# Optimization experiments

Measured on AMD Instinct MI355X. Metric: run time of the kernel, lower is better.

## Reference

```python
import jax, jax.numpy as jnp
import numpy as np
import math

H = 8  # num_heads
SCALE = 1.0 / math.sqrt(512.0)  # original divides by sqrt(dim_V), not sqrt(head_dim)


def setup_inputs() -> dict:
    key = jax.random.key(0)
    ks = jax.random.split(key, 16)
    B, N, D = 32, 512, 512
    s = 1.0 / math.sqrt(D)
    return {
        "Q": jax.random.normal(ks[0], (B, N, D), jnp.float32),
        "K": jax.random.normal(ks[1], (B, N, D), jnp.float32),
        "Wq": jax.random.normal(ks[2], (D, D), jnp.float32) * s,
        "bq": jnp.zeros((D,), jnp.float32),
        "Wk": jax.random.normal(ks[3], (D, D), jnp.float32) * s,
        "bk": jnp.zeros((D,), jnp.float32),
        "Wv": jax.random.normal(ks[4], (D, D), jnp.float32) * s,
        "bv": jnp.zeros((D,), jnp.float32),
        "Wo": jax.random.normal(ks[5], (D, D), jnp.float32) * s,
        "bo": jnp.zeros((D,), jnp.float32),
        "W1": jax.random.normal(ks[6], (D, D), jnp.float32) * s,
        "b1": jnp.zeros((D,), jnp.float32),
        "W2": jax.random.normal(ks[7], (D, D), jnp.float32) * s,
        "b2": jnp.zeros((D,), jnp.float32),
    }


def reference(Q, K, Wq, bq, Wk, bk, Wv, bv, Wo, bo, W1, b1, W2, b2):
    B, Nq, D = Q.shape
    dh = D // H
    # projections (torch Linear: x @ W.T + b)
    q = (Q @ Wq.T + bq).reshape(B, Nq, H, dh)
    k = (K @ Wk.T + bk).reshape(B, K.shape[1], H, dh)
    v = (K @ Wv.T + bv).reshape(B, K.shape[1], H, dh)
    # scores: [B, H, Nq, Nk], scaled by 1/sqrt(dim_V)
    scores = jnp.einsum("bqhd,bkhd->bhqk", q, k) * SCALE
    # NOTE: original softmax is over dim=1 of [H*B, Nq, Nk] == the QUERY axis
    A = jax.nn.softmax(scores, axis=2)
    attn = jnp.einsum("bhqk,bkhd->bqhd", A, v).reshape(B, Nq, D)
    out = Q + (attn @ Wo.T + bo)  # dropout p=0.0
    ffn = jax.nn.relu(out @ W1.T + b1) @ W2.T + b2
    return out + ffn
```

## Files before the change

kernel.cpp:

```cpp
#include <hip/hip_runtime.h>
#include <stdint.h>

#define SCALE_ 0.044194173824159216f
#define QSC_ (0.044194173824159216f * 1.4426950408889634f)

typedef __attribute__((ext_vector_type(8))) short bf16x8;
typedef __attribute__((ext_vector_type(4))) float f32x4;
typedef __attribute__((ext_vector_type(16))) float f32x16;
typedef __attribute__((ext_vector_type(2))) unsigned int uint2v;

__device__ __forceinline__ ushort f2b(float f) {
  union { float f; uint32_t u; } v; v.f = f;
  return (ushort)((v.u + 0x7fffu + ((v.u >> 16) & 1u)) >> 16);
}
__device__ __forceinline__ uint32_t cvtpk(float lo, float hi) {
  uint32_t r; asm("v_cvt_pk_bf16_f32 %0, %1, %2" : "=v"(r) : "v"(lo), "v"(hi)); return r;
}
__device__ __forceinline__ float ex2(float x) {
  float r; asm("v_exp_f32 %0, %1" : "=v"(r) : "v"(x)); return r;
}
__device__ __forceinline__ void gld16(void* lds, const void* g) {
  __builtin_amdgcn_global_load_lds(
      (const __attribute__((address_space(1))) uint32_t*)g,
      (__attribute__((address_space(3))) uint32_t*)lds, 16, 0, 0);
}

__global__ __launch_bounds__(256)
void k_cvtw(const float* __restrict__ w0, const float* __restrict__ w1,
            const float* __restrict__ w2, const float* __restrict__ w3,
            const float* __restrict__ w4, const float* __restrict__ w5,
            ushort* __restrict__ Wb)
{
  const int NW = 262144;
  int i = (blockIdx.x * 256 + threadIdx.x) * 4;
  int seg = i >> 18;
  int off = i & (NW - 1);
  const float* src;
  switch (seg) { case 0: src = w0; break; case 1: src = w1; break; case 2: src = w2; break;
                 case 3: src = w3; break; case 4: src = w4; break; default: src = w5; }
  float4 v = *(const float4*)(src + off);
  ushort4 o = make_ushort4(f2b(v.x), f2b(v.y), f2b(v.z), f2b(v.w));
  *(ushort4*)(Wb + (size_t)seg * NW + off) = o;
}

template<int EPI>
__device__ __forceinline__ void gemm_body(const ushort* __restrict__ A, const ushort* __restrict__ Bw,
                                          const float* __restrict__ bias, const float* __restrict__ extra,
                                          float* __restrict__ outf, ushort* __restrict__ outb,
                                          char* lds, int m0, int n0)
{
  const int t = threadIdx.x;
  const int w = t >> 6, lane = t & 63;
  const int wm = w >> 1, wn = w & 1;
  const int rA = lane & 15, g = lane >> 4;

  const ushort* srcA[4]; int ldsA[4];
#pragma unroll
  for (int j = 0; j < 4; j++) {
    int L = (t + j*512) * 16;
    int U = L ^ (((L >> 7) & 7) << 4);
    srcA[j] = A + (size_t)(m0 + (U >> 7))*512 + ((U & 127) >> 1);
    ldsA[j] = L;
  }
  const ushort* srcB[2]; int ldsB[2];
#pragma unroll
  for (int j = 0; j < 2; j++) {
    int L = (t + j*512) * 16;
    int U = L ^ (((L >> 7) & 7) << 4);
    srcB[j] = Bw + (size_t)(n0 + (U >> 7))*512 + ((U & 127) >> 1);
    ldsB[j] = 32768 + L;
  }

#define STAGE_A(ti) do { char* bb_ = lds + ((ti) % 3) * 49152; \
    _Pragma("unroll") \
    for (int j = 0; j < 4; j++) gld16(bb_ + ldsA[j], srcA[j] + (ti)*64); } while (0)
#define STAGE_B(ti) do { char* bb_ = lds + ((ti) % 3) * 49152; \
    _Pragma("unroll") \
    for (int j = 0; j < 2; j++) gld16(bb_ + ldsB[j], srcB[j] + (ti)*64); } while (0)

  STAGE_A(0); STAGE_B(0);
  STAGE_A(1); STAGE_B(1);

  f32x4 acc[4][4] = {};
  for (int i = 0; i < 8; i++) {
    if (i < 7) asm volatile("s_waitcnt vmcnt(6)" ::: "memory");
    else       asm volatile("s_waitcnt vmcnt(0)" ::: "memory");
    __builtin_amdgcn_s_barrier();
    __builtin_amdgcn_sched_barrier(0);
    const char* bufc = lds + (i % 3) * 49152;

    bf16x8 afA[4], bfA[4], afB[4], bfB[4];
#pragma unroll
    for (int m = 0; m < 4; m++) {
      int row = wm*64 + m*16 + rA;
      afA[m] = *(const bf16x8*)(bufc + ((row*128 + g*16) ^ ((row & 7) << 4)));
      afB[m] = *(const bf16x8*)(bufc + ((row*128 + 64 + g*16) ^ ((row & 7) << 4)));
    }
#pragma unroll
    for (int n = 0; n < 4; n++) {
      int row = wn*64 + n*16 + rA;
      bfA[n] = *(const bf16x8*)(bufc + 32768 + ((row*128 + g*16) ^ ((row & 7) << 4)));
      bfB[n] = *(const bf16x8*)(bufc + 32768 + ((row*128 + 64 + g*16) ^ ((row & 7) << 4)));
    }
    if (i < 6) { STAGE_A(i + 2); STAGE_B(i + 2); }
    __builtin_amdgcn_sched_barrier(0);
    __builtin_amdgcn_s_setprio(1);
#pragma unroll
    for (int m = 0; m < 4; m++)
#pragma unroll
      for (int n = 0; n < 4; n++)
        acc[m][n] = __builtin_amdgcn_mfma_f32_16x16x32_bf16(afA[m], bfA[n], acc[m][n], 0, 0, 0);
#pragma unroll
    for (int m = 0; m < 4; m++)
#pragma unroll
      for (int n = 0; n < 4; n++)
        acc[m][n] = __builtin_amdgcn_mfma_f32_16x16x32_bf16(afB[m], bfB[n], acc[m][n], 0, 0, 0);
    __builtin_amdgcn_s_setprio(0);
  }
#undef STAGE_A
#undef STAGE_B

#pragma unroll
  for (int m = 0; m < 4; m++)
#pragma unroll
    for (int n = 0; n < 4; n++) {
      int col = n0 + wn*64 + n*16 + rA;
      float bb = bias[col];
#pragma unroll
      for (int r = 0; r < 4; r++) {
        int row = m0 + wm*64 + m*16 + g*4 + r;
        size_t idx = (size_t)row*512 + col;
        float v = acc[m][n][r] + bb;
        if (EPI == 1)      { float o = extra[idx] + v; outf[idx] = o; outb[idx] = f2b(o); }
        else if (EPI == 2) outb[idx] = f2b(v > 0.f ? v : 0.f);
        else               outf[idx] += v;
      }
    }
}

template<int EPI>
__global__ __launch_bounds__(512, 2)
void k_gemm(const ushort* __restrict__ A, const ushort* __restrict__ Bw,
            const float* __restrict__ bias, const float* __restrict__ extra,
            float* __restrict__ outf, ushort* __restrict__ outb)
{
  __shared__ __align__(16) char lds[3*49152];
  gemm_body<EPI>(A, Bw, bias, extra, outf, outb, lds, blockIdx.x*256, blockIdx.y*128);
}

template<int EPI>
__device__ __forceinline__ void gemm_f32a_body(const float* __restrict__ A32, const ushort* __restrict__ Bw,
                                               const float* __restrict__ bias,
                                               float* __restrict__ outf, ushort* __restrict__ outb,
                                               char* lds, int m0, int n0, float os)
{
  const int t = threadIdx.x;
  const int w = t >> 6, lane = t & 63;
  const int wm = w >> 1, wn = w & 1;
  const int rA = lane & 15, g = lane >> 4;

  const float* srcA[4]; int ldsA[4];
#pragma unroll
  for (int j = 0; j < 4; j++) {
    int L = (t + j*512) * 16;
    int U = L ^ (((L >> 7) & 7) << 4);
    srcA[j] = A32 + (size_t)(m0 + (U >> 7))*512 + ((U & 127) >> 1);
    ldsA[j] = L;
  }
  const ushort* srcB[2]; int ldsB[2];
#pragma unroll
  for (int j = 0; j < 2; j++) {
    int L = (t + j*512) * 16;
    int U = L ^ (((L >> 7) & 7) << 4);
    srcB[j] = Bw + (size_t)(n0 + (U >> 7))*512 + ((U & 127) >> 1);
    ldsB[j] = 32768 + L;
  }

#define QLA(ti, R) do { \
    _Pragma("unroll") \
    for (int j = 0; j < 4; j++) { \
      R[2*j]   = *(const float4*)(srcA[j] + (ti)*64); \
      R[2*j+1] = *(const float4*)(srcA[j] + (ti)*64 + 4); } } while (0)
#define QWA(ti, R) do { char* bb_ = lds + ((ti) % 3) * 49152; \
    _Pragma("unroll") \
    for (int j = 0; j < 4; j++) { \
      uint4 qq; \
      qq.x = cvtpk(R[2*j].x,   R[2*j].y); \
      qq.y = cvtpk(R[2*j].z,   R[2*j].w); \
      qq.z = cvtpk(R[2*j+1].x, R[2*j+1].y); \
      qq.w = cvtpk(R[2*j+1].z, R[2*j+1].w); \
      *(uint4*)(bb_ + ldsA[j]) = qq; } } while (0)
#define QSB(ti) do { char* bb_ = lds + ((ti) % 3) * 49152; \
    _Pragma("unroll") \
    for (int j = 0; j < 2; j++) gld16(bb_ + ldsB[j], srcB[j] + (ti)*64); } while (0)

  float4 a0[8], a1[8], a2[8];
  QSB(0);
  QLA(0, a0);
  QLA(1, a1);
  QLA(2, a2);
  QSB(1);
  __builtin_amdgcn_sched_barrier(0);
  asm volatile("s_waitcnt vmcnt(18)" ::: "memory");
  QWA(0, a0);

  f32x4 acc[4][4] = {};

#define QITER(i, RW, RL) do { \
    if ((i) <= 5)      asm volatile("s_waitcnt vmcnt(10) lgkmcnt(0)" ::: "memory"); \
    else if ((i) == 6) asm volatile("s_waitcnt vmcnt(2) lgkmcnt(0)" ::: "memory"); \
    else               asm volatile("s_waitcnt vmcnt(0) lgkmcnt(0)" ::: "memory"); \
    __builtin_amdgcn_s_barrier(); \
    __builtin_amdgcn_sched_barrier(0); \
    if ((i) < 7) QWA((i) + 1, RW); \
    __builtin_amdgcn_sched_barrier(0); \
    const char* bufc = lds + ((i) % 3) * 49152; \
    bf16x8 afA[4], bfA[4]; \
    _Pragma("unroll") \
    for (int m = 0; m < 4; m++) { \
      int row = wm*64 + m*16 + rA; \
      afA[m] = *(const bf16x8*)(bufc + ((row*128 + g*16) ^ ((row & 7) << 4))); \
    } \
    _Pragma("unroll") \
    for (int n = 0; n < 4; n++) { \
      int row = wn*64 + n*16 + rA; \
      bfA[n] = *(const bf16x8*)(bufc + 32768 + ((row*128 + g*16) ^ ((row & 7) << 4))); \
    } \
    if ((i) < 5) QLA((i) + 3, RL); \
    if ((i) < 6) QSB((i) + 2); \
    __builtin_amdgcn_sched_barrier(0); \
    __builtin_amdgcn_s_setprio(1); \
    _Pragma("unroll") \
    for (int m = 0; m < 4; m++) \
      _Pragma("unroll") \
      for (int n = 0; n < 4; n++) \
        acc[m][n] = __builtin_amdgcn_mfma_f32_16x16x32_bf16(afA[m], bfA[n], acc[m][n], 0, 0, 0); \
    __builtin_amdgcn_s_setprio(0); \
    bf16x8 afB[4], bfB[4]; \
    _Pragma("unroll") \
    for (int m = 0; m < 4; m++) { \
      int row = wm*64 + m*16 + rA; \
      afB[m] = *(const bf16x8*)(bufc + ((row*128 + 64 + g*16) ^ ((row & 7) << 4))); \
    } \
    _Pragma("unroll") \
    for (int n = 0; n < 4; n++) { \
      int row = wn*64 + n*16 + rA; \
      bfB[n] = *(const bf16x8*)(bufc + 32768 + ((row*128 + 64 + g*16) ^ ((row & 7) << 4))); \
    } \
    __builtin_amdgcn_s_setprio(1); \
    _Pragma("unroll") \
    for (int m = 0; m < 4; m++) \
      _Pragma("unroll") \
      for (int n = 0; n < 4; n++) \
        acc[m][n] = __builtin_amdgcn_mfma_f32_16x16x32_bf16(afB[m], bfB[n], acc[m][n], 0, 0, 0); \
    __builtin_amdgcn_s_setprio(0); \
  } while (0)

  QITER(0, a1, a0);
  QITER(1, a2, a1);
  QITER(2, a0, a2);
  QITER(3, a1, a0);
  QITER(4, a2, a1);
  QITER(5, a0, a2);
  QITER(6, a1, a0);
  QITER(7, a2, a1);
#undef QITER
#undef QLA
#undef QWA
#undef QSB

#pragma unroll
  for (int m = 0; m < 4; m++)
#pragma unroll
    for (int n = 0; n < 4; n++) {
      int col = n0 + wn*64 + n*16 + rA;
      float bb = bias[col];
      if (EPI == 4) {
        int b = m0 >> 9, k0 = m0 & 511;
        int hh = col >> 6, dl = col & 63;
        int kg = k0 + wm*64 + m*16 + g*4;
        float v0 = acc[m][n][0] + bb, v1 = acc[m][n][1] + bb;
        float v2 = acc[m][n][2] + bb, v3 = acc[m][n][3] + bb;
        uint2 pk;
        pk.x = (uint32_t)f2b(v0) | ((uint32_t)f2b(v1) << 16);
        pk.y = (uint32_t)f2b(v2) | ((uint32_t)f2b(v3) << 16);
        *(uint2*)(outb + ((size_t)((b*8 + hh)*64 + dl)*512 + kg)) = pk;
      } else {
#pragma unroll
        for (int r = 0; r < 4; r++) {
          int row = m0 + wm*64 + m*16 + g*4 + r;
          size_t idx = (size_t)row*512 + col;
          outb[idx] = f2b((acc[m][n][r] + bb) * os);
        }
      }
    }
}

__global__ __launch_bounds__(512, 2)
void k_gemm_qkvf(const float* __restrict__ Qf, const float* __restrict__ Kf,
                 const ushort* __restrict__ Wb, const float* __restrict__ bq,
                 const float* __restrict__ bk, const float* __restrict__ bvv,
                 ushort* __restrict__ qkout, ushort* __restrict__ vpT)
{
  __shared__ __align__(16) char lds[3*49152];
  int z = blockIdx.z;
  if (z == 2) {
    gemm_f32a_body<4>(Kf, Wb + 2*(size_t)262144, bvv, nullptr, vpT,
                      lds, blockIdx.x*256, blockIdx.y*128, 1.0f);
  } else if (z == 1) {
    gemm_f32a_body<0>(Kf, Wb + (size_t)262144, bk, nullptr, qkout + (size_t)8388608,
                      lds, blockIdx.x*256, blockIdx.y*128, 1.0f);
  } else {
    gemm_f32a_body<0>(Qf, Wb, bq, nullptr, qkout,
                      lds, blockIdx.x*256, blockIdx.y*128, QSC_);
  }
}

__global__ __launch_bounds__(512, 2)
void k_att2(const ushort* __restrict__ qp, const ushort* __restrict__ kp,
            const ushort* __restrict__ vpT, float* __restrict__ zinv,
            ushort* __restrict__ attn)
{
  __shared__ __align__(16) char kt[65536];
  __shared__ __align__(16) char vt[65536];
  __shared__ __align__(16) char qpr[32768];
  int bh = blockIdx.x;
  int b = bh >> 3, h = bh & 7;
  int t = threadIdx.x, w = t >> 6, lane = t & 63;
  int rA = lane & 15, g = lane >> 4;
  const ushort* kbase = kp + (size_t)(b*512)*512 + h*64;
  const ushort* qbase = qp + (size_t)(b*512)*512 + h*64;
  const ushort* vbase = vpT + (size_t)bh*64*512;

#pragma unroll
  for (int i = 0; i < 8; i++) {
    int c = i*512 + t; int row = c >> 3, sl = c & 7;
    gld16(kt + c*16, kbase + (size_t)row*512 + ((sl ^ (row & 7))*8));
  }
#define STAGE_Q(buf, qb) do { \
    _Pragma("unroll") \
    for (int i = 0; i < 2; i++) { \
      int c = i*512 + t; int row = c >> 3, sl = c & 7; \
      gld16(qpr + (buf)*16384 + c*16, \
            qbase + (size_t)((qb)*128 + row)*512 + ((sl ^ (row & 7))*8)); } } while (0)
  STAGE_Q(0, 0);
  STAGE_Q(1, 1);
#pragma unroll
  for (int i = 0; i < 8; i++) {
    int c = i*512 + t; int d = c >> 6, sl = c & 63;
    gld16(vt + c*16, vbase + (size_t)d*512 + ((sl ^ (d & 7))*8));
  }

  asm volatile("s_waitcnt vmcnt(10)" ::: "memory");
  __builtin_amdgcn_s_barrier();
  __builtin_amdgcn_sched_barrier(0);
  bf16x8 kf[4][2];
#pragma unroll
  for (int n = 0; n < 4; n++)
#pragma unroll
    for (int ks = 0; ks < 2; ks++) {
      int k = w*64 + n*16 + rA;
      kf[n][ks] = *(const bf16x8*)(kt + k*128 + (((ks*4 + g) ^ (k & 7))*16));
    }
  float Zacc[4] = {0.f, 0.f, 0.f, 0.f};
  for (int qb = 0; qb < 4; qb++) {
    if (qb == 1)      { asm volatile("s_waitcnt vmcnt(10)" ::: "memory"); }
    else if (qb == 2) { asm volatile("s_waitcnt vmcnt(2)" ::: "memory"); }
    else if (qb == 3) { asm volatile("s_waitcnt vmcnt(0)" ::: "memory"); }
    if (qb) { __builtin_amdgcn_s_barrier(); __builtin_amdgcn_sched_barrier(0); }
    const char* qtb = qpr + (qb & 1)*16384;
    f32x4 acc[8][4] = {};
#pragma unroll
    for (int ks = 0; ks < 2; ks++) {
      bf16x8 af[8];
#pragma unroll
      for (int m = 0; m < 8; m++) {
        int q = m*16 + rA;
        af[m] = *(const bf16x8*)(qtb + q*128 + (((ks*4 + g) ^ (q & 7))*16));
      }
      __builtin_amdgcn_s_setprio(1);
#pragma unroll
      for (int m = 0; m < 8; m++)
#pragma unroll
        for (int n = 0; n < 4; n++)
          acc[m][n] = __builtin_amdgcn_mfma_f32_16x16x32_bf16(af[m], kf[n][ks], acc[m][n], 0, 0, 0);
      __builtin_amdgcn_s_setprio(0);
    }
    if (qb < 3) __builtin_amdgcn_s_barrier();
    if (qb < 2) STAGE_Q(qb & 1, qb + 2);
#pragma unroll
    for (int m = 0; m < 8; m++)
#pragma unroll
      for (int n = 0; n < 4; n++) {
        float s = 0.f;
#pragma unroll
        for (int r = 0; r < 4; r++) s += ex2(acc[m][n][r]);
        Zacc[n] += s;
      }
  }
#undef STAGE_Q
#pragma unroll
  for (int n = 0; n < 4; n++) {
    float v = Zacc[n];
    v += __shfl_xor(v, 16);
    v += __shfl_xor(v, 32);
    if (lane < 16) ((float*)qpr)[w*64 + n*16 + lane] = 1.0f / v;
  }
  __syncthreads();

  const int l31 = lane & 31, hi5 = lane >> 5;
  bf16x8 qf2[2][4];
#pragma unroll
  for (int qb = 0; qb < 2; qb++)
#pragma unroll
    for (int ksd = 0; ksd < 4; ksd++)
      qf2[qb][ksd] = *(const bf16x8*)(qbase + (size_t)(w*64 + qb*32 + l31)*512 + ksd*16 + hi5*8);
  const float* zl = (const float*)qpr;
  f32x16 oacc[2][2] = {};
  for (int kc = 0; kc < 16; kc++) {
    bf16x8 kf2[4];
#pragma unroll
    for (int ksd = 0; ksd < 4; ksd++) {
      int k = kc*32 + l31;
      kf2[ksd] = *(const bf16x8*)(kt + k*128 + (((ksd*2 + hi5) ^ (k & 7))*16));
    }
    bf16x8 vf2[2][2];
#pragma unroll
    for (int db = 0; db < 2; db++)
#pragma unroll
      for (int ks = 0; ks < 2; ks++) {
        int d = db*32 + l31;
        vf2[db][ks] = *(const bf16x8*)(vt + d*1024 + (((kc*4 + ks*2 + hi5) ^ (d & 7))*16));
      }
    f32x4 zv[4];
#pragma unroll
    for (int j = 0; j < 4; j++)
      zv[j] = *(const f32x4*)(zl + kc*32 + j*8 + hi5*4);
#pragma unroll
    for (int qb = 0; qb < 2; qb++) {
      f32x16 s = {};
      __builtin_amdgcn_s_setprio(1);
#pragma unroll
      for (int ksd = 0; ksd < 4; ksd++)
        s = __builtin_amdgcn_mfma_f32_32x32x16_bf16(kf2[ksd], qf2[qb][ksd], s, 0, 0, 0);
      __builtin_amdgcn_s_setprio(0);
      float e[16];
#pragma unroll
      for (int r = 0; r < 16; r++) e[r] = ex2(s[r]) * zv[r >> 2][r & 3];
      uint32_t x0 = cvtpk(e[0], e[1]),   y0 = cvtpk(e[4], e[5]);
      uint32_t x1 = cvtpk(e[2], e[3]),   y1 = cvtpk(e[6], e[7]);
      uint32_t x2 = cvtpk(e[8], e[9]),   y2 = cvtpk(e[12], e[13]);
      uint32_t x3 = cvtpk(e[10], e[11]), y3 = cvtpk(e[14], e[15]);
      uint2v r0 = __builtin_amdgcn_permlane32_swap(x0, y0, false, false);
      uint2v r1 = __builtin_amdgcn_permlane32_swap(x1, y1, false, false);
      uint2v r2 = __builtin_amdgcn_permlane32_swap(x2, y2, false, false);
      uint2v r3 = __builtin_amdgcn_permlane32_swap(x3, y3, false, false);
      union { uint32_t u[4]; bf16x8 v; } p0, p1;
      p0.u[0] = r0[0]; p0.u[1] = r1[0]; p0.u[2] = r0[1]; p0.u[3] = r1[1];
      p1.u[0] = r2[0]; p1.u[1] = r3[0]; p1.u[2] = r2[1]; p1.u[3] = r3[1];
      __builtin_amdgcn_s_setprio(1);
#pragma unroll
      for (int db = 0; db < 2; db++) {
        oacc[qb][db] = __builtin_amdgcn_mfma_f32_32x32x16_bf16(p0.v, vf2[db][0], oacc[qb][db], 0, 0, 0);
        oacc[qb][db] = __builtin_amdgcn_mfma_f32_32x32x16_bf16(p1.v, vf2[db][1], oacc[qb][db], 0, 0, 0);
      }
      __builtin_amdgcn_s_setprio(0);
    }
  }
#pragma unroll
  for (int qb = 0; qb < 2; qb++)
#pragma unroll
    for (int db = 0; db < 2; db++)
#pragma unroll
      for (int r = 0; r < 16; r++) {
        int q = w*64 + qb*32 + (r & 3) + 8*(r >> 2) + 4*hi5;
        int d = db*32 + l31;
        attn[(size_t)(b*512 + q)*512 + h*64 + d] = f2b(oacc[qb][db][r]);
      }
}

extern "C" void kernel_launch(void* const* d_in, const int* in_sizes, int n_in,
                              void* d_out, int out_size, void* d_ws, size_t ws_size,
                              hipStream_t stream) {
  const float* Q  = (const float*)d_in[0];
  const float* K  = (const float*)d_in[1];
  const float* Wq = (const float*)d_in[2];
  const float* bq = (const float*)d_in[3];
  const float* Wk = (const float*)d_in[4];
  const float* bk = (const float*)d_in[5];
  const float* Wv = (const float*)d_in[6];
  const float* bv = (const float*)d_in[7];
  const float* Wo = (const float*)d_in[8];
  const float* bo = (const float*)d_in[9];
  const float* W1 = (const float*)d_in[10];
  const float* b1 = (const float*)d_in[11];
  const float* W2 = (const float*)d_in[12];
  const float* b2 = (const float*)d_in[13];
  float* out = (float*)d_out;

  const size_t SZ = (size_t)16384 * 512;
  ushort* attn = (ushort*)d_ws;
  ushort* outb = attn + SZ;
  ushort* qp   = outb + SZ;
  ushort* kp   = qp + SZ;
  ushort* vpT  = kp + SZ;
  ushort* Wb   = vpT + SZ;
  float*  zinv = (float*)(Wb + 6 * (size_t)262144);
  ushort* h1   = vpT;

  k_cvtw<<<dim3(1536), dim3(256), 0, stream>>>(Wq, Wk, Wv, Wo, W1, W2, Wb);
  k_gemm_qkvf<<<dim3(64, 4, 3), dim3(512), 0, stream>>>(Q, K, Wb, bq, bk, bv, qp, vpT);
  k_att2<<<dim3(256), dim3(512), 0, stream>>>(qp, kp, vpT, zinv, attn);
  k_gemm<1><<<dim3(64, 4), dim3(512), 0, stream>>>(attn, Wb + 3*(size_t)262144, bo, Q, out, outb);
  k_gemm<2><<<dim3(64, 4), dim3(512), 0, stream>>>(outb, Wb + 4*(size_t)262144, b1, nullptr, nullptr, h1);
  k_gemm<3><<<dim3(64, 4), dim3(512), 0, stream>>>(h1, Wb + 5*(size_t)262144, b2, nullptr, out, nullptr);
}
```

Baseline: 146.5 us.

## Split fused attention kernel into column-normalizer and PV kernels

Splits the single attention kernel into two. k_z computes the per-key softmax normalizers over the query axis using 512 blocks of 256 threads, each handling half the keys of a (batch, head) with smaller LDS. k_pv then loads K, V and the precomputed normalizers and does the weighted P·V pass. The goal is higher occupancy and parallelism for the normalizer phase, which was serialized inside one 256-block kernel, at the cost of an extra launch, a global round trip for zinv, and reloading K.

```diff
diff --git a/kernel.cpp b/kernel.cpp
--- a/kernel.cpp
+++ b/kernel.cpp
@@ -316,59 +316,38 @@
   }
 }
 
-__global__ __launch_bounds__(512, 2)
-void k_att2(const ushort* __restrict__ qp, const ushort* __restrict__ kp,
-            const ushort* __restrict__ vpT, float* __restrict__ zinv,
-            ushort* __restrict__ attn)
-{
-  __shared__ __align__(16) char kt[65536];
-  __shared__ __align__(16) char vt[65536];
-  __shared__ __align__(16) char qpr[32768];
-  int bh = blockIdx.x;
+__global__ __launch_bounds__(256, 2)
+void k_z(const ushort* __restrict__ qp, const ushort* __restrict__ kp, float* __restrict__ zinv)
+{
+  __shared__ __align__(16) ushort qt[2*8192];
+  int bid = blockIdx.x;
+  int bh = bid >> 1, kh = bid & 1;
   int b = bh >> 3, h = bh & 7;
   int t = threadIdx.x, w = t >> 6, lane = t & 63;
   int rA = lane & 15, g = lane >> 4;
-  const ushort* kbase = kp + (size_t)(b*512)*512 + h*64;
   const ushort* qbase = qp + (size_t)(b*512)*512 + h*64;
-  const ushort* vbase = vpT + (size_t)bh*64*512;
-
-#pragma unroll
-  for (int i = 0; i < 8; i++) {
-    int c = i*512 + t; int row = c >> 3, sl = c & 7;
-    gld16(kt + c*16, kbase + (size_t)row*512 + ((sl ^ (row & 7))*8));
-  }
-#define STAGE_Q(buf, qb) do { \
-    _Pragma("unroll") \
-    for (int i = 0; i < 2; i++) { \
-      int c = i*512 + t; int row = c >> 3, sl = c & 7; \
-      gld16(qpr + (buf)*16384 + c*16, \
+  bf16x8 kf[4][2];
+#pragma unroll
+  for (int n = 0; n < 4; n++)
+#pragma unroll
+    for (int ks = 0; ks < 2; ks++)
+      kf[n][ks] = *(const bf16x8*)(kp + (size_t)(b*512 + kh*256 + w*64 + n*16 + rA)*512 + h*64 + ks*32 + g*8);
+
+#define Z_STAGE(buf, qb) do { \
+    _Pragma("unroll") \
+    for (int i = 0; i < 4; i++) { \
+      int c = i*256 + w*64 + lane; \
+      int row = c >> 3, sl = c & 7; \
+      gld16((char*)qt + (buf)*16384 + i*4096 + w*1024, \
             qbase + (size_t)((qb)*128 + row)*512 + ((sl ^ (row & 7))*8)); } } while (0)
-  STAGE_Q(0, 0);
-  STAGE_Q(1, 1);
-#pragma unroll
-  for (int i = 0; i < 8; i++) {
-    int c = i*512 + t; int d = c >> 6, sl = c & 63;
-    gld16(vt + c*16, vbase + (size_t)d*512 + ((sl ^ (d & 7))*8));
-  }
-
-  asm volatile("s_waitcnt vmcnt(10)" ::: "memory");
-  __builtin_amdgcn_s_barrier();
-  __builtin_amdgcn_sched_barrier(0);
-  bf16x8 kf[4][2];
-#pragma unroll
-  for (int n = 0; n < 4; n++)
-#pragma unroll
-    for (int ks = 0; ks < 2; ks++) {
-      int k = w*64 + n*16 + rA;
-      kf[n][ks] = *(const bf16x8*)(kt + k*128 + (((ks*4 + g) ^ (k & 7))*16));
-    }
+
+  Z_STAGE(0, 0);
+  __syncthreads();
   float Zacc[4] = {0.f, 0.f, 0.f, 0.f};
   for (int qb = 0; qb < 4; qb++) {
-    if (qb == 1)      { asm volatile("s_waitcnt vmcnt(10)" ::: "memory"); }
-    else if (qb == 2) { asm volatile("s_waitcnt vmcnt(2)" ::: "memory"); }
-    else if (qb == 3) { asm volatile("s_waitcnt vmcnt(0)" ::: "memory"); }
-    if (qb) { __builtin_amdgcn_s_barrier(); __builtin_amdgcn_sched_barrier(0); }
-    const char* qtb = qpr + (qb & 1)*16384;
+    const int cur = qb & 1;
+    if (qb < 3) Z_STAGE(cur ^ 1, qb + 1);
+    const ushort* qtb = qt + cur*8192;
     f32x4 acc[8][4] = {};
 #pragma unroll
     for (int ks = 0; ks < 2; ks++) {
@@ -376,7 +355,7 @@
 #pragma unroll
       for (int m = 0; m < 8; m++) {
         int q = m*16 + rA;
-        af[m] = *(const bf16x8*)(qtb + q*128 + (((ks*4 + g) ^ (q & 7))*16));
+        af[m] = *(const bf16x8*)(qtb + q*64 + (((ks*4 + g) ^ (q & 7))*8));
       }
       __builtin_amdgcn_s_setprio(1);
 #pragma unroll
@@ -386,8 +365,6 @@
           acc[m][n] = __builtin_amdgcn_mfma_f32_16x16x32_bf16(af[m], kf[n][ks], acc[m][n], 0, 0, 0);
       __builtin_amdgcn_s_setprio(0);
     }
-    if (qb < 3) __builtin_amdgcn_s_barrier();
-    if (qb < 2) STAGE_Q(qb & 1, qb + 2);
 #pragma unroll
     for (int m = 0; m < 8; m++)
 #pragma unroll
@@ -397,16 +374,44 @@
         for (int r = 0; r < 4; r++) s += ex2(acc[m][n][r]);
         Zacc[n] += s;
       }
-  }
-#undef STAGE_Q
+    __syncthreads();
+  }
+#undef Z_STAGE
 #pragma unroll
   for (int n = 0; n < 4; n++) {
     float v = Zacc[n];
     v += __shfl_xor(v, 16);
     v += __shfl_xor(v, 32);
-    if (lane < 16) ((float*)qpr)[w*64 + n*16 + lane] = 1.0f / v;
-  }
-  __syncthreads();
+    if (lane < 16) zinv[(size_t)bh*512 + kh*256 + w*64 + n*16 + lane] = 1.0f / v;
+  }
+}
+
+__global__ __launch_bounds__(512, 2)
+void k_pv(const ushort* __restrict__ qp, const ushort* __restrict__ kp,
+          const ushort* __restrict__ vpT, const float* __restrict__ zinv,
+          ushort* __restrict__ attn)
+{
+  __shared__ __align__(16) char kt[65536];
+  __shared__ __align__(16) char vt[65536];
+  __shared__ __align__(16) float zl[512];
+  int bh = blockIdx.x;
+  int b = bh >> 3, h = bh & 7;
+  int t = threadIdx.x, w = t >> 6, lane = t & 63;
+  const ushort* kbase = kp + (size_t)(b*512)*512 + h*64;
+  const ushort* qbase = qp + (size_t)(b*512)*512 + h*64;
+  const ushort* vbase = vpT + (size_t)bh*64*512;
+
+#pragma unroll
+  for (int i = 0; i < 8; i++) {
+    int c = i*512 + t; int row = c >> 3, sl = c & 7;
+    gld16(kt + c*16, kbase + (size_t)row*512 + ((sl ^ (row & 7))*8));
+  }
+#pragma unroll
+  for (int i = 0; i < 8; i++) {
+    int c = i*512 + t; int d = c >> 6, sl = c & 63;
+    gld16(vt + c*16, vbase + (size_t)d*512 + ((sl ^ (d & 7))*8));
+  }
+  zl[t] = zinv[(size_t)bh*512 + t];
 
   const int l31 = lane & 31, hi5 = lane >> 5;
   bf16x8 qf2[2][4];
@@ -415,7 +420,11 @@
 #pragma unroll
     for (int ksd = 0; ksd < 4; ksd++)
       qf2[qb][ksd] = *(const bf16x8*)(qbase + (size_t)(w*64 + qb*32 + l31)*512 + ksd*16 + hi5*8);
-  const float* zl = (const float*)qpr;
+
+  asm volatile("s_waitcnt vmcnt(0) lgkmcnt(0)" ::: "memory");
+  __builtin_amdgcn_s_barrier();
+  __builtin_amdgcn_sched_barrier(0);
+
   f32x16 oacc[2][2] = {};
   for (int kc = 0; kc < 16; kc++) {
     bf16x8 kf2[4];
@@ -435,7 +444,7 @@
     f32x4 zv[4];
 #pragma unroll
     for (int j = 0; j < 4; j++)
-      zv[j] = *(const f32x4*)(zl + kc*32 + j*8 + hi5*4);
+      zv[j] = *(const f32x4*)(&zl[kc*32 + j*8 + hi5*4]);
 #pragma unroll
     for (int qb = 0; qb < 2; qb++) {
       f32x16 s = {};
@@ -510,7 +519,8 @@
 
   k_cvtw<<<dim3(1536), dim3(256), 0, stream>>>(Wq, Wk, Wv, Wo, W1, W2, Wb);
   k_gemm_qkvf<<<dim3(64, 4, 3), dim3(512), 0, stream>>>(Q, K, Wb, bq, bk, bv, qp, vpT);
-  k_att2<<<dim3(256), dim3(512), 0, stream>>>(qp, kp, vpT, zinv, attn);
+  k_z<<<dim3(512), dim3(256), 0, stream>>>(qp, kp, zinv);
+  k_pv<<<dim3(256), dim3(512), 0, stream>>>(qp, kp, vpT, zinv, attn);
   k_gemm<1><<<dim3(64, 4), dim3(512), 0, stream>>>(attn, Wb + 3*(size_t)262144, bo, Q, out, outb);
   k_gemm<2><<<dim3(64, 4), dim3(512), 0, stream>>>(outb, Wb + 4*(size_t)262144, b1, nullptr, nullptr, h1);
   k_gemm<3><<<dim3(64, 4), dim3(512), 0, stream>>>(h1, Wb + 5*(size_t)262144, b2, nullptr, out, nullptr);
```

Result: slower. 154.2 us (+5.2%).
